# Optimization experiments

Measured on AMD Instinct MI355X. Metric: run time of the kernel, lower is better.

## Reference

```python
import jax, jax.numpy as jnp
import numpy as np

D = 768
H = 8
HD = D // H
FF = 4 * D


def _linear_params(key, din, dout):
    kw, kb = jax.random.split(key)
    lim = 1.0 / np.sqrt(din)
    W = jax.random.uniform(kw, (din, dout), jnp.float32, -lim, lim)
    b = jax.random.uniform(kb, (dout,), jnp.float32, -lim, lim)
    return W, b


def setup_inputs() -> dict:
    key = jax.random.key(0)
    ks = jax.random.split(key, 8)
    x = jax.random.normal(ks[0], (16, 1024, D), jnp.float32)
    Wq, bq = _linear_params(ks[1], D, D)
    Wk, bk = _linear_params(ks[2], D, D)
    Wv, bv = _linear_params(ks[3], D, D)
    Wo, bo = _linear_params(ks[4], D, D)
    W1, b1 = _linear_params(ks[5], D, FF)
    W2, b2 = _linear_params(ks[6], FF, D)
    gamma = jnp.ones((D,), jnp.float32)
    beta = jnp.zeros((D,), jnp.float32)
    return {"x": x, "gamma": gamma, "beta": beta,
            "Wq": Wq, "bq": bq, "Wk": Wk, "bk": bk, "Wv": Wv, "bv": bv,
            "Wo": Wo, "bo": bo, "W1": W1, "b1": b1, "W2": W2, "b2": b2}


def _layernorm(x, gamma, beta, eps=1e-5):
    mu = jnp.mean(x, axis=-1, keepdims=True)
    var = jnp.var(x, axis=-1, keepdims=True)
    return (x - mu) * jax.lax.rsqrt(var + eps) * gamma + beta


def _block(x, gamma, beta, Wq, bq, Wk, bk, Wv, bv, Wo, bo, W1, b1, W2, b2):
    b, n, d = x.shape
    residual = x
    h = _layernorm(x, gamma, beta)
    # QKV projections -> [b, h, n, hd]
    q = (h @ Wq + bq).reshape(b, n, H, HD).transpose(0, 2, 1, 3)
    k = (h @ Wk + bk).reshape(b, n, H, HD).transpose(0, 2, 1, 3)
    v = (h @ Wv + bv).reshape(b, n, H, HD).transpose(0, 2, 1, 3)
    scale = HD ** 0.5
    scores = jnp.einsum('bhid,bhjd->bhij', q, k) / scale
    attn = jax.nn.softmax(scores, axis=-1)
    out = jnp.einsum('bhij,bhjd->bhid', attn, v)
    out = out.transpose(0, 2, 1, 3).reshape(b, n, d)
    out = out @ Wo + bo
    out = out + residual
    residual = out
    h = _layernorm(out, gamma, beta)  # same LN params reused (as in source)
    h = jax.nn.gelu(h @ W1 + b1, approximate=False)
    h = h @ W2 + b2
    return h + residual


def reference(x, gamma, beta, Wq, bq, Wk, bk, Wv, bv, Wo, bo, W1, b1, W2, b2):
    return _block(x, gamma, beta, Wq, bq, Wk, bk, Wv, bv, Wo, bo, W1, b1, W2, b2)
```

## Files before the change

kernel.cpp:

```cpp
#include <hip/hip_runtime.h>

typedef unsigned short u16;
typedef float f32x4 __attribute__((ext_vector_type(4)));
typedef __bf16 bf16x8 __attribute__((ext_vector_type(8)));

#define AS1 __attribute__((address_space(1)))
#define AS3 __attribute__((address_space(3)))

__device__ __forceinline__ float bf2f(u16 h) {
  return __uint_as_float(((unsigned)h) << 16);
}
__device__ __forceinline__ u16 f2bf(float f) {
  unsigned u = __float_as_uint(f);
  unsigned r = (u + 0x7FFFu + ((u >> 16) & 1u)) >> 16;
  return (u16)r;
}
__device__ __forceinline__ void gload16(const u16* g, u16* l) {
  __builtin_amdgcn_global_load_lds((const AS1 void*)g, (AS3 void*)l, 16, 0, 0);
}

__global__ void transpose_k(const float* __restrict__ in, u16* __restrict__ out,
                            int R, int C) {
  __shared__ u16 t[32][33];
  int c0 = blockIdx.x * 32, r0 = blockIdx.y * 32;
  int tx = threadIdx.x & 31, ty = threadIdx.x >> 5;
  for (int i = 0; i < 32; i += 8)
    t[ty + i][tx] = f2bf(in[(size_t)(r0 + ty + i) * C + c0 + tx]);
  __syncthreads();
  for (int i = 0; i < 32; i += 8)
    out[(size_t)(c0 + ty + i) * R + r0 + tx] = t[tx][ty + i];
}

__global__ void transpose4_k(const float* __restrict__ s0, const float* __restrict__ s1,
                             const float* __restrict__ s2, const float* __restrict__ s3,
                             u16* __restrict__ d0, u16* __restrict__ d1,
                             u16* __restrict__ d2, u16* __restrict__ d3) {
  __shared__ u16 t[32][33];
  const float* in = (blockIdx.z == 0) ? s0 : (blockIdx.z == 1) ? s1
                    : (blockIdx.z == 2) ? s2 : s3;
  u16* out = (blockIdx.z == 0) ? d0 : (blockIdx.z == 1) ? d1
             : (blockIdx.z == 2) ? d2 : d3;
  int c0 = blockIdx.x * 32, r0 = blockIdx.y * 32;
  int tx = threadIdx.x & 31, ty = threadIdx.x >> 5;
  for (int i = 0; i < 32; i += 8)
    t[ty + i][tx] = f2bf(in[(size_t)(r0 + ty + i) * 768 + c0 + tx]);
  __syncthreads();
  for (int i = 0; i < 32; i += 8)
    out[(size_t)(c0 + ty + i) * 768 + r0 + tx] = t[tx][ty + i];
}

__global__ void pack3_k(const float* __restrict__ a, const float* __restrict__ b,
                        const float* __restrict__ c, float* __restrict__ out) {
  int i = blockIdx.x * 256 + threadIdx.x;
  float v = (i < 768) ? a[i] : (i < 1536) ? b[i - 768] : c[i - 1536];
  out[i] = v;
}

__global__ void vtrans_k(const u16* __restrict__ v, u16* __restrict__ vt) {
  __shared__ u16 t[32][33];
  int bh = blockIdx.z, b = bh >> 3, h = bh & 7;
  int n0 = blockIdx.y * 32, d0 = blockIdx.x * 32;
  int tx = threadIdx.x & 31, ty = threadIdx.x >> 5;
  const u16* src = v + (size_t)(b * 1024) * 768 + h * 96;
  for (int i = 0; i < 32; i += 8)
    t[ty + i][tx] = src[(size_t)(n0 + ty + i) * 768 + d0 + tx];
  __syncthreads();
  u16* dst = vt + ((size_t)bh * 96 + d0) * 1024 + n0;
  for (int i = 0; i < 32; i += 8)
    dst[(size_t)(ty + i) * 1024 + tx] = t[tx][ty + i];
}

__global__ __launch_bounds__(256) void ln_f32_k(const float* __restrict__ x,
                                                const float* __restrict__ gamma,
                                                const float* __restrict__ beta,
                                                u16* __restrict__ out) {
  __shared__ float red[8];
  int row = blockIdx.x, t = threadIdx.x;
  const float* xr = x + (size_t)row * 768;
  float v[3], s = 0.f, s2 = 0.f;
#pragma unroll
  for (int i = 0; i < 3; i++) {
    v[i] = xr[t + i * 256];
    s += v[i]; s2 += v[i] * v[i];
  }
#pragma unroll
  for (int off = 1; off < 64; off <<= 1) {
    s += __shfl_xor(s, off, 64);
    s2 += __shfl_xor(s2, off, 64);
  }
  int w = t >> 6;
  if ((t & 63) == 0) { red[w] = s; red[4 + w] = s2; }
  __syncthreads();
  s = red[0] + red[1] + red[2] + red[3];
  s2 = red[4] + red[5] + red[6] + red[7];
  float mu = s * (1.f / 768.f);
  float var = s2 * (1.f / 768.f) - mu * mu;
  float rs = rsqrtf(var + 1e-5f);
  u16* orow = out + (size_t)row * 768;
#pragma unroll
  for (int i = 0; i < 3; i++) {
    int c = t + i * 256;
    orow[c] = f2bf((v[i] - mu) * rs * gamma[c] + beta[c]);
  }
}

#define BM 128
#define BN 128
#define BK 64

template <int EPI>
__global__ __launch_bounds__(256, 4) void gemm_bt(
    const u16* __restrict__ A, const u16* __restrict__ Bt,
    const float* __restrict__ bias, const float* __restrict__ res,
    void* __restrict__ Cv, int M, int N, int K, int lda) {
  __shared__ u16 As[BM * BK];
  __shared__ u16 Bs[BN * BK];
  int tid = threadIdx.x, lane = tid & 63, w = tid >> 6;
  int l15 = lane & 15, quad = lane >> 4;
  int wm = (w >> 1) * 64, wn = (w & 1) * 64;
  int GX = gridDim.x;
  int f = blockIdx.y * GX + blockIdx.x;
  int mpx = GX >> 3;
  int xcd = f & 7, idx = f >> 3;
  int m0 = (xcd * mpx + (idx % mpx)) * BM;
  int n0 = (idx / mpx) * BN;
  int NT = K / BK;
  int sr[4], sc[4];
#pragma unroll
  for (int i = 0; i < 4; i++) {
    int c = w * 4 + i;
    sr[i] = (c >> 1) * 16 + l15;
    sc[i] = (c & 1) * 32 + quad * 8;
  }
  f32x4 acc[4][4] = {};
  for (int t = 0; t < NT; t++) {
    __syncthreads();
    int k0 = t * BK;
#pragma unroll
    for (int i = 0; i < 4; i++) {
      int c = w * 4 + i;
      gload16(A + (size_t)(m0 + sr[i]) * lda + k0 + sc[i], As + c * 512);
      gload16(Bt + (size_t)(n0 + sr[i]) * K + k0 + sc[i], Bs + c * 512);
    }
    __syncthreads();
#pragma unroll
    for (int kk = 0; kk < 2; kk++) {
      bf16x8 af[4], bfv[4];
#pragma unroll
      for (int i = 0; i < 4; i++) {
        int ga = (w >> 1) * 4 + i;
        int gb = (w & 1) * 4 + i;
        af[i] = *(const bf16x8*)(As + (ga * 2 + kk) * 512 + lane * 8);
        bfv[i] = *(const bf16x8*)(Bs + (gb * 2 + kk) * 512 + lane * 8);
      }
#pragma unroll
      for (int mt = 0; mt < 4; mt++)
#pragma unroll
        for (int nt = 0; nt < 4; nt++)
          acc[mt][nt] = __builtin_amdgcn_mfma_f32_16x16x32_bf16(
              af[mt], bfv[nt], acc[mt][nt], 0, 0, 0);
    }
  }
#pragma unroll
  for (int nt = 0; nt < 4; nt++) {
    int col = n0 + wn + nt * 16 + l15;
    float bv = bias[col];
#pragma unroll
    for (int mt = 0; mt < 4; mt++) {
      int row = m0 + wm + mt * 16 + quad * 4;
#pragma unroll
      for (int r = 0; r < 4; r++) {
        float v = acc[mt][nt][r] + bv;
        size_t idx2 = (size_t)(row + r) * N + col;
        if (EPI == 4) {
          v += res[idx2];
          ((float*)Cv)[idx2] = v;
        } else {
          if (EPI == 2) v = 0.5f * v * (1.0f + erff(v * 0.70710678118654752f));
          ((u16*)Cv)[idx2] = f2bf(v);
        }
      }
    }
  }
}

template <int EPI>
__global__ __launch_bounds__(512, 4) void gemm512_bt(
    const u16* __restrict__ A, const u16* __restrict__ Bt,
    const float* __restrict__ bias, const float* __restrict__ res,
    void* __restrict__ Cv, int M, int N, int K, int lda) {
  __shared__ u16 As[2][256 * 64];
  __shared__ u16 Bs[2][64 * 64];
  int tid = threadIdx.x, lane = tid & 63, w = tid >> 6;
  int l15 = lane & 15, quad = lane >> 4;
  int wr = w >> 1, wc = w & 1;
  int GX = gridDim.x;
  int f = blockIdx.y * GX + blockIdx.x;
  int mpx = GX >> 3;
  int xcd = f & 7, idx = f >> 3;
  int m0 = (xcd * mpx + (idx % mpx)) * 256;
  int n0 = (idx / mpx) * 64;
  int NT = K / 64;
#pragma unroll
  for (int i = 0; i < 4; i++) {
    int c = w * 4 + i;
    gload16(A + (size_t)(m0 + (c >> 1) * 16 + l15) * lda + (c & 1) * 32 + quad * 8,
            As[0] + c * 512);
  }
  gload16(Bt + (size_t)(n0 + (w >> 1) * 16 + l15) * K + (w & 1) * 32 + quad * 8,
          Bs[0] + w * 512);
  f32x4 acc[4][2] = {};
  for (int t = 0; t < NT; t++) {
    int cur = t & 1;
    int k0 = (t + 1 < NT) ? (t + 1) * 64 : 0;
#pragma unroll
    for (int i = 0; i < 4; i++) {
      int c = w * 4 + i;
      gload16(A + (size_t)(m0 + (c >> 1) * 16 + l15) * lda + k0 + (c & 1) * 32 + quad * 8,
              As[cur ^ 1] + c * 512);
    }
    gload16(Bt + (size_t)(n0 + (w >> 1) * 16 + l15) * K + k0 + (w & 1) * 32 + quad * 8,
            Bs[cur ^ 1] + w * 512);
    asm volatile("s_waitcnt vmcnt(5)" ::: "memory");
    __builtin_amdgcn_s_barrier();
    const u16* ab = As[cur];
    const u16* bb = Bs[cur];
#pragma unroll
    for (int kk = 0; kk < 2; kk++) {
      bf16x8 af[4], bfv[2];
#pragma unroll
      for (int i = 0; i < 4; i++) {
        int rg = wr * 4 + i;
        af[i] = *(const bf16x8*)(ab + (rg * 2 + kk) * 512 + lane * 8);
      }
#pragma unroll
      for (int i = 0; i < 2; i++) {
        int rg = wc * 2 + i;
        bfv[i] = *(const bf16x8*)(bb + (rg * 2 + kk) * 512 + lane * 8);
      }
#pragma unroll
      for (int mt = 0; mt < 4; mt++)
#pragma unroll
        for (int nt = 0; nt < 2; nt++)
          acc[mt][nt] = __builtin_amdgcn_mfma_f32_16x16x32_bf16(
              af[mt], bfv[nt], acc[mt][nt], 0, 0, 0);
    }
    __builtin_amdgcn_s_barrier();
  }
  asm volatile("s_waitcnt vmcnt(0)" ::: "memory");
  int seg = (EPI == 1) ? (n0 >= 1536 ? 2 : (n0 >= 768 ? 1 : 0)) : 0;
#pragma unroll
  for (int nt = 0; nt < 2; nt++) {
    int col = n0 + wc * 32 + nt * 16 + l15;
    float bv = bias[col];
#pragma unroll
    for (int mt = 0; mt < 4; mt++) {
      int row = m0 + wr * 64 + mt * 16 + quad * 4;
#pragma unroll
      for (int r = 0; r < 4; r++) {
        float v = acc[mt][nt][r] + bv;
        if (EPI == 1) {
          u16* outp = (u16*)Cv + (size_t)seg * 16384 * 768;
          outp[(size_t)(row + r) * 768 + (col - seg * 768)] = f2bf(v);
        } else {
          size_t idx2 = (size_t)(row + r) * N + col;
          if (EPI == 4) {
            v += res[idx2];
            ((float*)Cv)[idx2] = v;
          } else {
            if (EPI == 2) v = 0.5f * v * (1.0f + erff(v * 0.70710678118654752f));
            ((u16*)Cv)[idx2] = f2bf(v);
          }
        }
      }
    }
  }
}

#define QSS 104
#define VSS 72
#define PSS 72
__global__ __launch_bounds__(256, 2) void attn_k(const u16* __restrict__ q,
                                                 const u16* __restrict__ k,
                                                 const u16* __restrict__ vt,
                                                 u16* __restrict__ o) {
  __shared__ u16 qs[64 * QSS];
  __shared__ u16 ks[2][64 * QSS];
  __shared__ u16 vts[2][96 * VSS];
  __shared__ u16 ps[4 * 16 * PSS];
  int tid = threadIdx.x, lane = tid & 63, w = tid >> 6;
  int l15 = lane & 15, quad = lane >> 4;
  int f = blockIdx.y * 16 + blockIdx.x;
  int xcd = f & 7, idx = f >> 3;
  int bh = xcd * 16 + (idx & 15);
  int qt = idx >> 4;
  int b = bh >> 3, h = bh & 7;
  const u16* qbase = q + (size_t)(b * 1024 + qt * 64) * 768 + h * 96;
  const u16* kbase = k + (size_t)(b * 1024) * 768 + h * 96;
  const u16* vtbase = vt + (size_t)bh * 96 * 1024;
  int kr[3], ko[3], vr[3], vo[3];
#pragma unroll
  for (int i = 0; i < 3; i++) {
    int c = tid + i * 256;
    kr[i] = c / 12; ko[i] = (c % 12) * 8;
    vr[i] = c >> 3; vo[i] = (c & 7) * 8;
  }
#pragma unroll
  for (int i = 0; i < 3; i++)
    *(uint4*)(qs + kr[i] * QSS + ko[i]) =
        *(const uint4*)(qbase + (size_t)kr[i] * 768 + ko[i]);
  uint4 kreg[3], vreg[3];
#pragma unroll
  for (int i = 0; i < 3; i++) {
    kreg[i] = *(const uint4*)(kbase + (size_t)kr[i] * 768 + ko[i]);
    vreg[i] = *(const uint4*)(vtbase + (size_t)vr[i] * 1024 + vo[i]);
  }
#pragma unroll
  for (int i = 0; i < 3; i++) {
    *(uint4*)(ks[0] + kr[i] * QSS + ko[i]) = kreg[i];
    *(uint4*)(vts[0] + vr[i] * VSS + vo[i]) = vreg[i];
  }
  __syncthreads();

  float mi[4], li[4];
#pragma unroll
  for (int r = 0; r < 4; r++) { mi[r] = -1e30f; li[r] = 0.f; }
  f32x4 oacc[6] = {};
  const float scale = 0.10206207261596577f;
  for (int kt = 0; kt < 16; kt++) {
    int cur = kt & 1, nxt = cur ^ 1;
    int ktn = (kt + 1) & 15;
#pragma unroll
    for (int i = 0; i < 3; i++) {
      kreg[i] = *(const uint4*)(kbase + (size_t)(ktn * 64 + kr[i]) * 768 + ko[i]);
      vreg[i] = *(const uint4*)(vtbase + (size_t)vr[i] * 1024 + ktn * 64 + vo[i]);
    }
    f32x4 s[4] = {};
#pragma unroll
    for (int kk = 0; kk < 3; kk++) {
      bf16x8 a = *(const bf16x8*)(qs + (w * 16 + l15) * QSS + kk * 32 + quad * 8);
#pragma unroll
      for (int nt = 0; nt < 4; nt++) {
        bf16x8 bb =
            *(const bf16x8*)(ks[cur] + (nt * 16 + l15) * QSS + kk * 32 + quad * 8);
        s[nt] = __builtin_amdgcn_mfma_f32_16x16x32_bf16(a, bb, s[nt], 0, 0, 0);
      }
    }
#pragma unroll
    for (int r = 0; r < 4; r++) {
      float sv[4], mx = -1e30f;
#pragma unroll
      for (int nt = 0; nt < 4; nt++) {
        sv[nt] = s[nt][r];
        mx = fmaxf(mx, sv[nt]);
      }
#pragma unroll
      for (int off = 1; off < 16; off <<= 1) mx = fmaxf(mx, __shfl_xor(mx, off, 16));
      float mnew = fmaxf(mi[r], mx);
      float alpha = __expf((mi[r] - mnew) * scale);
      float rs = 0.f;
#pragma unroll
      for (int nt = 0; nt < 4; nt++) {
        sv[nt] = __expf((sv[nt] - mnew) * scale);
        rs += sv[nt];
      }
      li[r] = li[r] * alpha + rs;
      mi[r] = mnew;
#pragma unroll
      for (int ht = 0; ht < 6; ht++) oacc[ht][r] *= alpha;
      int prow = quad * 4 + r;
#pragma unroll
      for (int nt = 0; nt < 4; nt++)
        ps[w * 16 * PSS + prow * PSS + nt * 16 + l15] = f2bf(sv[nt]);
    }
    asm volatile("s_waitcnt lgkmcnt(0)" ::: "memory");
#pragma unroll
    for (int kk = 0; kk < 2; kk++) {
      bf16x8 a = *(const bf16x8*)(ps + w * 16 * PSS + l15 * PSS + kk * 32 + quad * 8);
#pragma unroll
      for (int ht = 0; ht < 6; ht++) {
        bf16x8 bb =
            *(const bf16x8*)(vts[cur] + (ht * 16 + l15) * VSS + kk * 32 + quad * 8);
        oacc[ht] = __builtin_amdgcn_mfma_f32_16x16x32_bf16(a, bb, oacc[ht], 0, 0, 0);
      }
    }
#pragma unroll
    for (int i = 0; i < 3; i++) {
      *(uint4*)(ks[nxt] + kr[i] * QSS + ko[i]) = kreg[i];
      *(uint4*)(vts[nxt] + vr[i] * VSS + vo[i]) = vreg[i];
    }
    __syncthreads();
  }
#pragma unroll
  for (int r = 0; r < 4; r++)
#pragma unroll
    for (int off = 1; off < 16; off <<= 1) li[r] += __shfl_xor(li[r], off, 16);
  u16* obase = o + (size_t)(b * 1024 + qt * 64 + w * 16) * 768 + h * 96;
#pragma unroll
  for (int r = 0; r < 4; r++) {
    float inv = 1.0f / li[r];
    int row = quad * 4 + r;
#pragma unroll
    for (int ht = 0; ht < 6; ht++)
      obase[(size_t)row * 768 + ht * 16 + l15] = f2bf(oacc[ht][r] * inv);
  }
}

extern "C" void kernel_launch(void* const* d_in, const int* in_sizes, int n_in,
                              void* d_out, int out_size, void* d_ws,
                              size_t ws_size, hipStream_t stream) {
  const float* x = (const float*)d_in[0];
  const float* gamma = (const float*)d_in[1];
  const float* beta = (const float*)d_in[2];
  const float* Wq = (const float*)d_in[3];
  const float* bq = (const float*)d_in[4];
  const float* Wk = (const float*)d_in[5];
  const float* bk = (const float*)d_in[6];
  const float* Wv = (const float*)d_in[7];
  const float* bv = (const float*)d_in[8];
  const float* Wo = (const float*)d_in[9];
  const float* bo = (const float*)d_in[10];
  const float* W1 = (const float*)d_in[11];
  const float* b1 = (const float*)d_in[12];
  const float* W2 = (const float*)d_in[13];
  const float* b2 = (const float*)d_in[14];
  float* out = (float*)d_out;

  char* ws = (char*)d_ws;
  size_t off = 0;
  auto alloc = [&](size_t elems) {
    u16* p = (u16*)(ws + off);
    off += elems * sizeof(u16);
    return p;
  };
  u16* WqT = alloc(768 * 768);
  u16* WkT = alloc(768 * 768);
  u16* WvT = alloc(768 * 768);
  u16* WoT = alloc(768 * 768);
  u16* W1T = alloc((size_t)768 * 3072);
  u16* W2T = alloc((size_t)3072 * 768);
  float* bqkv = (float*)(ws + off); off += 2304 * sizeof(float);
  u16* hb = alloc((size_t)16384 * 768);
  u16* qb = alloc((size_t)16384 * 768);
  u16* kb = alloc((size_t)16384 * 768);
  u16* vb = alloc((size_t)16384 * 768);
  u16* vtb = (u16*)d_out;

  transpose4_k<<<dim3(24, 24, 4), 256, 0, stream>>>(Wq, Wk, Wv, Wo,
                                                    WqT, WkT, WvT, WoT);
  transpose_k<<<dim3(96, 24), 256, 0, stream>>>(W1, W1T, 768, 3072);
  transpose_k<<<dim3(24, 96), 256, 0, stream>>>(W2, W2T, 3072, 768);
  pack3_k<<<9, 256, 0, stream>>>(bq, bk, bv, bqkv);

  ln_f32_k<<<16384, 256, 0, stream>>>(x, gamma, beta, hb);
  gemm512_bt<1><<<dim3(64, 36), 512, 0, stream>>>(hb, WqT, bqkv, nullptr, qb,
                                                  16384, 2304, 768, 768);
  vtrans_k<<<dim3(3, 32, 128), 256, 0, stream>>>(vb, vtb);
  attn_k<<<dim3(16, 128), 256, 0, stream>>>(qb, kb, vtb, vb);
  gemm512_bt<4><<<dim3(64, 12), 512, 0, stream>>>(vb, WoT, bo, x, out,
                                                  16384, 768, 768, 768);
  ln_f32_k<<<16384, 256, 0, stream>>>(out, gamma, beta, kb);
  u16* fbuf = hb;
  for (int c = 0; c < 2; c++) {
    const u16* h2c = kb + (size_t)c * 8192 * 768;
    const float* y1c = out + (size_t)c * 8192 * 768;
    float* outc = out + (size_t)c * 8192 * 768;
    gemm512_bt<2><<<dim3(32, 48), 512, 0, stream>>>(h2c, W1T, b1, nullptr,
                                                    fbuf, 8192, 3072, 768, 768);
    gemm_bt<4><<<dim3(64, 6), 256, 0, stream>>>(fbuf, W2T, b2, y1c, outc,
                                                8192, 768, 3072, 3072);
  }
}
```

Measured before the change: 931.3 us.

## Replace 256x64 GEMM with 256x256 eight-wave ping-pong pipelined kernel for QKV and FFN1

Swaps the 256x64 tiled GEMM used for the QKV and first FFN projections for a 256x256 tile kernel. It uses 8 waves, two-deep LDS buffering staged in quarter-tiles interleaved with four MFMA phases, and s_setprio around the MFMA bursts. Larger tiles raise arithmetic intensity and cut redundant A loads. The trade is 128KB of LDS per block and fewer blocks per CU. The output projection moves to the existing 256-thread gemm_bt kernel.

```diff
diff --git a/kernel.cpp b/kernel.cpp
--- a/kernel.cpp
+++ b/kernel.cpp
@@ -185,92 +185,105 @@
 }
 
 template <int EPI>
-__global__ __launch_bounds__(512, 4) void gemm512_bt(
+__global__ __launch_bounds__(512, 2) void gemm8p_bt(
     const u16* __restrict__ A, const u16* __restrict__ Bt,
     const float* __restrict__ bias, const float* __restrict__ res,
     void* __restrict__ Cv, int M, int N, int K, int lda) {
-  __shared__ u16 As[2][256 * 64];
-  __shared__ u16 Bs[2][64 * 64];
+  __shared__ u16 lds_[2 * 32768];
   int tid = threadIdx.x, lane = tid & 63, w = tid >> 6;
   int l15 = lane & 15, quad = lane >> 4;
-  int wr = w >> 1, wc = w & 1;
+  int wr = w >> 2, wc = w & 3;
   int GX = gridDim.x;
   int f = blockIdx.y * GX + blockIdx.x;
   int mpx = GX >> 3;
   int xcd = f & 7, idx = f >> 3;
   int m0 = (xcd * mpx + (idx % mpx)) * 256;
-  int n0 = (idx / mpx) * 64;
+  int n0 = (idx / mpx) * 256;
   int NT = K / 64;
-#pragma unroll
-  for (int i = 0; i < 4; i++) {
-    int c = w * 4 + i;
-    gload16(A + (size_t)(m0 + (c >> 1) * 16 + l15) * lda + (c & 1) * 32 + quad * 8,
-            As[0] + c * 512);
-  }
-  gload16(Bt + (size_t)(n0 + (w >> 1) * 16 + l15) * K + (w & 1) * 32 + quad * 8,
-          Bs[0] + w * 512);
-  f32x4 acc[4][2] = {};
+
+  auto stage = [&](int st_tile, int pos) {
+    int stt = st_tile >= NT ? st_tile - NT : st_tile;
+    int kb = stt * 64;
+    u16* dst = lds_ + (stt & 1) * 32768 + pos * 8192;
+#pragma unroll
+    for (int i = 0; i < 2; i++) {
+      int s = w + i * 8;
+      int rr = (s >> 1) * 16 + l15, cc = kb + (s & 1) * 32 + quad * 8;
+      if (pos < 2)
+        gload16(A + (size_t)(m0 + pos * 128 + rr) * lda + cc, dst + s * 512);
+      else
+        gload16(Bt + (size_t)(n0 + (pos - 2) * 128 + rr) * K + cc, dst + s * 512);
+    }
+  };
+
+  f32x4 acc[8][4] = {};
+  bf16x8 af[8], bf[4];
+
+  stage(0, 0); stage(0, 1); stage(0, 2); stage(0, 3);
+  stage(1, 0); stage(1, 2);
+  asm volatile("s_waitcnt vmcnt(4)" ::: "memory");
+  __builtin_amdgcn_s_barrier();
+
   for (int t = 0; t < NT; t++) {
-    int cur = t & 1;
-    int k0 = (t + 1 < NT) ? (t + 1) * 64 : 0;
-#pragma unroll
-    for (int i = 0; i < 4; i++) {
-      int c = w * 4 + i;
-      gload16(A + (size_t)(m0 + (c >> 1) * 16 + l15) * lda + k0 + (c & 1) * 32 + quad * 8,
-              As[cur ^ 1] + c * 512);
-    }
-    gload16(Bt + (size_t)(n0 + (w >> 1) * 16 + l15) * K + k0 + (w & 1) * 32 + quad * 8,
-            Bs[cur ^ 1] + w * 512);
-    asm volatile("s_waitcnt vmcnt(5)" ::: "memory");
-    __builtin_amdgcn_s_barrier();
-    const u16* ab = As[cur];
-    const u16* bb = Bs[cur];
-#pragma unroll
-    for (int kk = 0; kk < 2; kk++) {
-      bf16x8 af[4], bfv[2];
-#pragma unroll
-      for (int i = 0; i < 4; i++) {
-        int rg = wr * 4 + i;
-        af[i] = *(const bf16x8*)(ab + (rg * 2 + kk) * 512 + lane * 8);
-      }
-#pragma unroll
-      for (int i = 0; i < 2; i++) {
-        int rg = wc * 2 + i;
-        bfv[i] = *(const bf16x8*)(bb + (rg * 2 + kk) * 512 + lane * 8);
-      }
-#pragma unroll
-      for (int mt = 0; mt < 4; mt++)
-#pragma unroll
-        for (int nt = 0; nt < 2; nt++)
-          acc[mt][nt] = __builtin_amdgcn_mfma_f32_16x16x32_bf16(
-              af[mt], bfv[nt], acc[mt][nt], 0, 0, 0);
-    }
-    __builtin_amdgcn_s_barrier();
+    const u16* abase = lds_ + (t & 1) * 32768 + wr * 8192;
+    const u16* bbase = lds_ + (t & 1) * 32768 + 16384 + (wc >> 1) * 8192;
+#pragma unroll
+    for (int p = 0; p < 4; p++) {
+      const int pm = p >> 1, pn = p & 1;
+      if (p == 0) stage(t + 1, 1);
+      else if (p == 1) stage(t + 1, 3);
+      else if (p == 2) stage(t + 2, 0);
+      else stage(t + 2, 2);
+      if (pn == 0) {
+#pragma unroll
+        for (int j = 0; j < 4; j++)
+#pragma unroll
+          for (int kk = 0; kk < 2; kk++)
+            af[j * 2 + kk] = *(const bf16x8*)(
+                abase + ((pm * 4 + j) * 2 + kk) * 512 + lane * 8);
+      }
+#pragma unroll
+      for (int j = 0; j < 2; j++)
+#pragma unroll
+        for (int kk = 0; kk < 2; kk++)
+          bf[j * 2 + kk] = *(const bf16x8*)(
+              bbase + (((wc & 1) * 4 + pn * 2 + j) * 2 + kk) * 512 + lane * 8);
+      if (p == 3) asm volatile("s_waitcnt vmcnt(4)" ::: "memory");
+      __builtin_amdgcn_s_barrier();
+      __builtin_amdgcn_s_setprio(1);
+#pragma unroll
+      for (int kk = 0; kk < 2; kk++)
+#pragma unroll
+        for (int j = 0; j < 4; j++)
+#pragma unroll
+          for (int n2 = 0; n2 < 2; n2++)
+            acc[pm * 4 + j][pn * 2 + n2] = __builtin_amdgcn_mfma_f32_16x16x32_bf16(
+                af[j * 2 + kk], bf[n2 * 2 + kk], acc[pm * 4 + j][pn * 2 + n2],
+                0, 0, 0);
+      __builtin_amdgcn_s_setprio(0);
+      __builtin_amdgcn_s_barrier();
+    }
   }
   asm volatile("s_waitcnt vmcnt(0)" ::: "memory");
-  int seg = (EPI == 1) ? (n0 >= 1536 ? 2 : (n0 >= 768 ? 1 : 0)) : 0;
-#pragma unroll
-  for (int nt = 0; nt < 2; nt++) {
-    int col = n0 + wc * 32 + nt * 16 + l15;
+
+  int seg = (EPI == 1) ? (n0 / 768) : 0;
+#pragma unroll
+  for (int ng = 0; ng < 4; ng++) {
+    int col = n0 + wc * 64 + ng * 16 + l15;
     float bv = bias[col];
 #pragma unroll
-    for (int mt = 0; mt < 4; mt++) {
-      int row = m0 + wr * 64 + mt * 16 + quad * 4;
+    for (int mg = 0; mg < 8; mg++) {
+      int row = m0 + wr * 128 + mg * 16 + quad * 4;
 #pragma unroll
       for (int r = 0; r < 4; r++) {
-        float v = acc[mt][nt][r] + bv;
+        float v = acc[mg][ng][r] + bv;
         if (EPI == 1) {
           u16* outp = (u16*)Cv + (size_t)seg * 16384 * 768;
           outp[(size_t)(row + r) * 768 + (col - seg * 768)] = f2bf(v);
         } else {
           size_t idx2 = (size_t)(row + r) * N + col;
-          if (EPI == 4) {
-            v += res[idx2];
-            ((float*)Cv)[idx2] = v;
-          } else {
-            if (EPI == 2) v = 0.5f * v * (1.0f + erff(v * 0.70710678118654752f));
-            ((u16*)Cv)[idx2] = f2bf(v);
-          }
+          if (EPI == 2) v = 0.5f * v * (1.0f + erff(v * 0.70710678118654752f));
+          ((u16*)Cv)[idx2] = f2bf(v);
         }
       }
     }
@@ -453,20 +466,20 @@
   pack3_k<<<9, 256, 0, stream>>>(bq, bk, bv, bqkv);
 
   ln_f32_k<<<16384, 256, 0, stream>>>(x, gamma, beta, hb);
-  gemm512_bt<1><<<dim3(64, 36), 512, 0, stream>>>(hb, WqT, bqkv, nullptr, qb,
-                                                  16384, 2304, 768, 768);
+  gemm8p_bt<1><<<dim3(64, 9), 512, 0, stream>>>(hb, WqT, bqkv, nullptr, qb,
+                                                16384, 2304, 768, 768);
   vtrans_k<<<dim3(3, 32, 128), 256, 0, stream>>>(vb, vtb);
   attn_k<<<dim3(16, 128), 256, 0, stream>>>(qb, kb, vtb, vb);
-  gemm512_bt<4><<<dim3(64, 12), 512, 0, stream>>>(vb, WoT, bo, x, out,
-                                                  16384, 768, 768, 768);
+  gemm_bt<4><<<dim3(128, 6), 256, 0, stream>>>(vb, WoT, bo, x, out,
+                                               16384, 768, 768, 768);
   ln_f32_k<<<16384, 256, 0, stream>>>(out, gamma, beta, kb);
   u16* fbuf = hb;
   for (int c = 0; c < 2; c++) {
     const u16* h2c = kb + (size_t)c * 8192 * 768;
     const float* y1c = out + (size_t)c * 8192 * 768;
     float* outc = out + (size_t)c * 8192 * 768;
-    gemm512_bt<2><<<dim3(32, 48), 512, 0, stream>>>(h2c, W1T, b1, nullptr,
-                                                    fbuf, 8192, 3072, 768, 768);
+    gemm8p_bt<2><<<dim3(32, 12), 512, 0, stream>>>(h2c, W1T, b1, nullptr,
+                                                   fbuf, 8192, 3072, 768, 768);
     gemm_bt<4><<<dim3(64, 6), 256, 0, stream>>>(fbuf, W2T, b2, y1c, outc,
                                                 8192, 768, 3072, 3072);
   }
```

Measured after the change: 851.3 us. -8.6%, faster.
